# Performance work log

Measured on AMD Instinct MI355X. Metric: run time of the kernel, lower is better.

Reference implementation:

```python
import jax, jax.numpy as jnp
import numpy as np

N = 131072          # total instances
G = 2048            # n_groups
MAX = 128           # padded max group size (>= true max by construction)
E = 256             # embed_dim
H = 8               # num_heads
D = E // H          # head dim


def setup_inputs() -> dict:
    key = jax.random.key(0)
    ks = jax.random.split(key, 9)
    # every group id appears at least once (matches torch.unique-derived groups)
    gids = jnp.concatenate([
        jnp.arange(G, dtype=jnp.int32),
        jax.random.randint(ks[0], (N - G,), 0, G, dtype=jnp.int32),
    ])
    return {
        "tree_preds": jax.random.normal(ks[1], (N, E), dtype=jnp.float32),
        "group_ids": gids,
        "query": jax.random.normal(ks[2], (1, 1, E), dtype=jnp.float32) * 0.02,
        "w_in": jax.random.normal(ks[3], (3 * E, E), dtype=jnp.float32) * 0.02,
        "b_in": jax.random.normal(ks[4], (3 * E,), dtype=jnp.float32) * 0.02,
        "w_out": jax.random.normal(ks[5], (E, E), dtype=jnp.float32) * 0.02,
        "b_out": jax.random.normal(ks[6], (E,), dtype=jnp.float32) * 0.02,
        "w_lin": jax.random.normal(ks[7], (1, E), dtype=jnp.float32) * 0.02,
        "b_lin": jax.random.normal(ks[8], (1,), dtype=jnp.float32) * 0.02,
    }


def _forward(tree_preds, group_ids, query, w_in, b_in, w_out, b_out, w_lin, b_lin):
    # --- scatter ragged groups into padded [G, MAX, E] tensor ---
    sorter = jnp.argsort(group_ids)                   # stable instance sorter
    sorted_gid = group_ids[sorter]
    sizes = jax.ops.segment_sum(jnp.ones_like(group_ids), group_ids,
                                num_segments=G)       # [G] group sizes
    offsets = jnp.cumsum(sizes) - sizes               # exclusive cumsum
    pos = jnp.arange(N, dtype=sizes.dtype) - offsets[sorted_gid]  # slot in group
    embs = jnp.zeros((G, MAX, E), dtype=tree_preds.dtype)
    embs = embs.at[sorted_gid, pos].set(tree_preds[sorter])
    kp_mask = jnp.arange(MAX)[None, :] >= sizes[:, None]          # [G, MAX] True=pad

    # --- single-query multi-head attention pooling ---
    wq, wk, wv = w_in[:E], w_in[E:2 * E], w_in[2 * E:]
    bq, bk, bv = b_in[:E], b_in[E:2 * E], b_in[2 * E:]
    q = (query.reshape(E) @ wq.T + bq).reshape(H, D)              # shared query
    k = (embs @ wk.T + bk).reshape(G, MAX, H, D)
    v = (embs @ wv.T + bv).reshape(G, MAX, H, D)
    scores = jnp.einsum("hd,gmhd->ghm", q, k) / jnp.sqrt(jnp.float32(D))
    scores = jnp.where(kp_mask[:, None, :], -jnp.inf, scores)
    attn = jax.nn.softmax(scores, axis=-1)                        # [G, H, MAX]
    pooled = jnp.einsum("ghm,gmhd->ghd", attn, v).reshape(G, E)
    pooled = pooled @ w_out.T + b_out                             # out_proj
    return pooled @ w_lin.T + b_lin                               # [G, 1]


def reference(tree_preds, group_ids, query, w_in, b_in, w_out, b_out, w_lin, b_lin):
    return _forward(tree_preds, group_ids, query, w_in, b_in,
                    w_out, b_out, w_lin, b_lin)
```

## Files before the change

### kernel.cpp

```cpp
#include <hip/hip_runtime.h>
#include <hip/hip_bf16.h>

#define EDIM 256
#define INV_SQRT_D 0.17677669529663688f
#define FXSCALE 1099511627776.0f

#define WS_QB   4096
#define WS_UB   4104
#define WS_C    4112
#define WS_QS   4128
#define WS_PU   4608
#define WB_BYTE_OFF 36864
#define ZM_BYTE_OFF 65536

typedef __attribute__((ext_vector_type(8))) short short8;
typedef __attribute__((ext_vector_type(4))) float f32x4;

__device__ __forceinline__ unsigned short f2bf(float f) {
  unsigned u = __float_as_uint(f);
  unsigned r = (u + 0x7fffu + ((u >> 16) & 1u)) >> 16;
  return (unsigned short)r;
}

__device__ __forceinline__ unsigned int cvt_pk_bf16(float a, float b) {
  __hip_bfloat162 t = __float22bfloat162_rn(float2{a, b});
  unsigned int u;
  __builtin_memcpy(&u, &t, 4);
  return u;
}

__global__ __launch_bounds__(256) void prep1(
    const float* __restrict__ query, const float* __restrict__ w_in,
    const float* __restrict__ b_in, const float* __restrict__ w_out,
    const float* __restrict__ w_lin, float* __restrict__ ws,
    unsigned long long* __restrict__ zm, int nzm) {
  const int b = blockIdx.x, t = threadIdx.x;
  if (b < 32) {
    const int r = b * 8 + (t >> 5);
    const int l = t & 31;
    const float4 q0 = *(const float4*)(query + l * 8);
    const float4 q1 = *(const float4*)(query + l * 8 + 4);
    const float4 w0 = *(const float4*)(w_in + (size_t)r * EDIM + l * 8);
    const float4 w1 = *(const float4*)(w_in + (size_t)r * EDIM + l * 8 + 4);
    float a = q0.x * w0.x + q0.y * w0.y + q0.z * w0.z + q0.w * w0.w
            + q1.x * w1.x + q1.y * w1.y + q1.z * w1.z + q1.w * w1.w;
    for (int m = 16; m >= 1; m >>= 1) a += __shfl_xor(a, m, 32);
    if (l == 0) ws[WS_QS + r] = a + b_in[r];
  } else if (b < 48) {
    const int k = b - 32;
    float acc = 0.f;
#pragma unroll
    for (int f = 0; f < 16; ++f) {
      const int fr = k * 16 + f;
      acc += w_lin[fr] * w_out[(size_t)fr * EDIM + t];
    }
    ws[WS_PU + k * EDIM + t] = acc;
  } else {
    for (int k = (b - 48) * 256 + t; k < nzm; k += 16 * 256) zm[k] = 0ull;
  }
}

__global__ __launch_bounds__(256) void prep2(
    const float* __restrict__ w_in, const float* __restrict__ b_in,
    const float* __restrict__ b_out, const float* __restrict__ b_lin,
    const float* __restrict__ w_lin, float* __restrict__ ws,
    unsigned short* __restrict__ wb) {
  const int b = blockIdx.x, t = threadIdx.x;
  if (b < 8) {
    __shared__ float qh[32];
    if (t < 32) qh[t] = ws[WS_QS + b * 32 + t];
    __syncthreads();
    float a = 0.f;
#pragma unroll 8
    for (int d = 0; d < 32; ++d)
      a += qh[d] * w_in[(size_t)(EDIM + b * 32 + d) * EDIM + t];
    wb[b * EDIM + t] = f2bf(a * INV_SQRT_D);
  } else if (b < 16) {
    const int j = b - 8;
    __shared__ float uh[32];
    if (t < 32) {
      float s = 0.f;
#pragma unroll
      for (int k = 0; k < 16; ++k) s += ws[WS_PU + k * EDIM + j * 32 + t];
      uh[t] = s;
    }
    __syncthreads();
    float a = 0.f;
#pragma unroll 8
    for (int d = 0; d < 32; ++d)
      a += uh[d] * w_in[(size_t)(2 * EDIM + j * 32 + d) * EDIM + t];
    wb[(8 + j) * EDIM + t] = f2bf(a);
  } else {
    __shared__ float us[EDIM];
    float s = 0.f;
#pragma unroll
    for (int k = 0; k < 16; ++k) s += ws[WS_PU + k * EDIM + t];
    us[t] = s;
    __syncthreads();
    if (t < 8) {
      float qb = 0.f, ub = 0.f;
#pragma unroll 4
      for (int d = 0; d < 32; ++d) {
        qb += ws[WS_QS + t * 32 + d] * b_in[EDIM + t * 32 + d];
        ub += us[t * 32 + d] * b_in[2 * EDIM + t * 32 + d];
      }
      ws[WS_QB + t] = qb * INV_SQRT_D;
      ws[WS_UB + t] = ub;
    }
    if (t == 0) {
      float c = b_lin[0];
      for (int f = 0; f < EDIM; ++f) c += w_lin[f] * b_out[f];
      ws[WS_C] = c;
    }
  }
}

__global__ __launch_bounds__(256, 4) void main_mfma(
    const float* __restrict__ x, const int* __restrict__ gid,
    const float* __restrict__ ws, const unsigned short* __restrict__ wb,
    unsigned long long* __restrict__ zm, int n_items) {
  const int t = threadIdx.x;
  const int lane = t & 63;
  const int n = lane & 15, quad = lane >> 4;
  const int h = n & 7, isw = (n >> 3) & 1;

  short8 bfrag[8];
#pragma unroll
  for (int kc = 0; kc < 8; ++kc)
    bfrag[kc] = *(const short8*)(wb + n * EDIM + quad * 8 + kc * 32);

  const float qb = ws[WS_QB + h];
  const float ub = ws[WS_UB + h];

  const int wid = (int)(blockIdx.x * (blockDim.x >> 6) + (t >> 6));
  const int nw = (int)(gridDim.x * (blockDim.x >> 6));
  const int ntiles = (n_items + 15) >> 4;

  for (int tile = wid; tile < ntiles; tile += nw) {
    const int base = tile << 4;
    const float* rowp = x + (size_t)(base + n) * EDIM + quad * 8;
    f32x4 acc = {0.f, 0.f, 0.f, 0.f};
    int4 g4;
    if (base + 16 <= n_items) {
      g4 = *(const int4*)(gid + base + quad * 4);
#pragma unroll
      for (int kc = 0; kc < 8; ++kc) {
        const float4 v0 = *(const float4*)(rowp + kc * 32);
        const float4 v1 = *(const float4*)(rowp + kc * 32 + 4);
        union { short8 s; unsigned int u[4]; } a;
        a.u[0] = cvt_pk_bf16(v0.x, v0.y);
        a.u[1] = cvt_pk_bf16(v0.z, v0.w);
        a.u[2] = cvt_pk_bf16(v1.x, v1.y);
        a.u[3] = cvt_pk_bf16(v1.z, v1.w);
        acc = __builtin_amdgcn_mfma_f32_16x16x32_bf16(a.s, bfrag[kc], acc, 0, 0, 0);
      }
    } else {
      int gg[4];
#pragma unroll
      for (int r = 0; r < 4; ++r)
        gg[r] = (base + quad * 4 + r < n_items) ? gid[base + quad * 4 + r] : 0;
      g4.x = gg[0]; g4.y = gg[1]; g4.z = gg[2]; g4.w = gg[3];
      const bool live = (base + n < n_items);
#pragma unroll
      for (int kc = 0; kc < 8; ++kc) {
        float4 v0 = {0.f, 0.f, 0.f, 0.f}, v1 = {0.f, 0.f, 0.f, 0.f};
        if (live) {
          v0 = *(const float4*)(rowp + kc * 32);
          v1 = *(const float4*)(rowp + kc * 32 + 4);
        }
        union { short8 s; unsigned int u[4]; } a;
        a.u[0] = cvt_pk_bf16(v0.x, v0.y);
        a.u[1] = cvt_pk_bf16(v0.z, v0.w);
        a.u[2] = cvt_pk_bf16(v1.x, v1.y);
        a.u[3] = cvt_pk_bf16(v1.z, v1.w);
        acc = __builtin_amdgcn_mfma_f32_16x16x32_bf16(a.s, bfrag[kc], acc, 0, 0, 0);
      }
    }
#pragma unroll
    for (int r = 0; r < 4; ++r) {
      const float mine = acc[r];
      const float partner = __shfl_xor(mine, 8, 64);
      const float sv = (isw ? partner : mine) + qb;
      const float wv = (isw ? mine : partner) + ub;
      const float e = __expf(sv);
      const float val = isw ? e * wv : e;
      const int g = (r == 0) ? g4.x : (r == 1) ? g4.y : (r == 2) ? g4.z : g4.w;
      if (base + quad * 4 + r < n_items) {
        const long long qv = llrintf(val * FXSCALE);
        atomicAdd(zm + ((size_t)g * 16 + h * 2 + isw), (unsigned long long)qv);
      }
    }
  }
}

__global__ __launch_bounds__(256) void finalize(
    const long long* __restrict__ zm, const float* __restrict__ ws,
    float* __restrict__ out, int G) {
  const int g = blockIdx.x * blockDim.x + threadIdx.x;
  if (g >= G) return;
  double acc = (double)ws[WS_C];
  const long long* row = zm + (size_t)g * 16;
#pragma unroll
  for (int hh = 0; hh < 8; ++hh)
    acc += (double)row[hh * 2 + 1] / (double)row[hh * 2];
  out[g] = (float)acc;
}

__device__ __forceinline__ float dot16_reduce(const float4 (&W)[16],
                                              const float4 xv, const int lane) {
  float p[16];
#pragma unroll
  for (int j = 0; j < 16; ++j)
    p[j] = W[j].x * xv.x + W[j].y * xv.y + W[j].z * xv.z + W[j].w * xv.w;
#pragma unroll
  for (int j = 0; j < 8; ++j) {
    float send = (lane & 1) ? p[j] : p[j + 8];
    float keep = (lane & 1) ? p[j + 8] : p[j];
    p[j] = keep + __shfl_xor(send, 1, 64);
  }
#pragma unroll
  for (int j = 0; j < 4; ++j) {
    float send = (lane & 2) ? p[j] : p[j + 4];
    float keep = (lane & 2) ? p[j + 4] : p[j];
    p[j] = keep + __shfl_xor(send, 2, 64);
  }
#pragma unroll
  for (int j = 0; j < 2; ++j) {
    float send = (lane & 4) ? p[j] : p[j + 2];
    float keep = (lane & 4) ? p[j + 2] : p[j];
    p[j] = keep + __shfl_xor(send, 4, 64);
  }
  {
    float send = (lane & 8) ? p[0] : p[1];
    float keep = (lane & 8) ? p[1] : p[0];
    p[0] = keep + __shfl_xor(send, 8, 64);
  }
  p[0] += __shfl_xor(p[0], 16, 64);
  p[0] += __shfl_xor(p[0], 32, 64);
  return p[0];
}

__device__ __forceinline__ int bitrev4(const int l4) {
  return ((l4 & 1) << 3) | ((l4 & 2) << 1) | ((l4 & 4) >> 1) | ((l4 & 8) >> 3);
}

__global__ __launch_bounds__(256) void group_scan(
    const float* __restrict__ x, const int* __restrict__ gid,
    const float* __restrict__ query, const float* __restrict__ w_in,
    const float* __restrict__ b_in, const float* __restrict__ w_out,
    const float* __restrict__ b_out, const float* __restrict__ w_lin,
    const float* __restrict__ b_lin, float* __restrict__ out, int n_items) {
  const int g = blockIdx.x;
  const int t = threadIdx.x;
  __shared__ float Wl[16 * EDIM];
  __shared__ float querys[EDIM], wls[EDIM], qs[EDIM], us[EDIM];
  __shared__ float qbias[8], ubias[8], csh;
  __shared__ float part[4][16], sums[16];

  querys[t] = query[t];
  wls[t] = w_lin[t];
  __syncthreads();
  {
    float acc = 0.f;
    const float4* wr = (const float4*)(w_in + (size_t)t * EDIM);
    for (int f4 = 0; f4 < EDIM / 4; ++f4) {
      float4 wv = wr[f4];
      int f = f4 * 4;
      acc += wv.x * querys[f] + wv.y * querys[f + 1] + wv.z * querys[f + 2] + wv.w * querys[f + 3];
    }
    qs[t] = acc + b_in[t];
  }
  {
    float acc = 0.f;
    for (int f = 0; f < EDIM; ++f) acc += wls[f] * w_out[(size_t)f * EDIM + t];
    us[t] = acc;
  }
  __syncthreads();
  for (int j = 0; j < 8; ++j) {
    float a = 0.f;
    for (int d = 0; d < 32; ++d)
      a += qs[j * 32 + d] * w_in[(size_t)(EDIM + j * 32 + d) * EDIM + t];
    Wl[j * EDIM + t] = a * INV_SQRT_D;
  }
  for (int j = 0; j < 8; ++j) {
    float a = 0.f;
    for (int d = 0; d < 32; ++d)
      a += us[j * 32 + d] * w_in[(size_t)(2 * EDIM + j * 32 + d) * EDIM + t];
    Wl[(8 + j) * EDIM + t] = a;
  }
  if (t < 8) {
    float qb = 0.f, ub = 0.f;
    for (int d = 0; d < 32; ++d) {
      qb += qs[t * 32 + d] * b_in[EDIM + t * 32 + d];
      ub += us[t * 32 + d] * b_in[2 * EDIM + t * 32 + d];
    }
    qbias[t] = qb * INV_SQRT_D;
    ubias[t] = ub;
  }
  if (t == 0) {
    float c = b_lin[0];
    for (int f = 0; f < EDIM; ++f) c += wls[f] * b_out[f];
    csh = c;
  }
  __syncthreads();

  const int lane = t & 63;
  const int wave = t >> 6;
  float4 W[16];
#pragma unroll
  for (int j = 0; j < 16; ++j)
    W[j] = *(const float4*)(Wl + j * EDIM + lane * 4);
  const int jv = bitrev4(lane & 15);
  const int h = jv & 7;
  const int isw = (jv >> 3) & 1;
  const float bias_s = qbias[h];
  const float bias_w = ubias[h];

  float accv = 0.f;
  const int nchunk = (n_items + 63) >> 6;
  for (int c = wave; c < nchunk; c += 4) {
    const int i0 = c << 6;
    const int ii = i0 + lane;
    const int gi = (ii < n_items) ? gid[ii] : -1;
    unsigned long long mk = __ballot(gi == g);
    while (mk) {
      const int bpos = __ffsll(mk) - 1;
      mk &= mk - 1;
      const int i = i0 + bpos;
      const float4 xv = *(const float4*)(x + (size_t)i * EDIM + lane * 4);
      const float p0 = dot16_reduce(W, xv, lane);
      const float tpair = __shfl_xor(p0, 1, 64);
      const float sv = (isw ? tpair : p0) + bias_s;
      const float wv = (isw ? p0 : tpair) + bias_w;
      const float e = __expf(sv);
      accv += isw ? e * wv : e;
    }
  }
  if (lane < 16) part[wave][h * 2 + isw] = accv;
  __syncthreads();
  if (t < 16) sums[t] = part[0][t] + part[1][t] + part[2][t] + part[3][t];
  __syncthreads();
  if (t == 0) {
    double acc = (double)csh;
    for (int hh = 0; hh < 8; ++hh)
      acc += (double)sums[2 * hh + 1] / (double)sums[2 * hh];
    out[g] = (float)acc;
  }
}

extern "C" void kernel_launch(void* const* d_in, const int* in_sizes, int n_in,
                              void* d_out, int out_size, void* d_ws, size_t ws_size,
                              hipStream_t stream) {
  const float* tree_preds = (const float*)d_in[0];
  const int* group_ids = (const int*)d_in[1];
  const float* query = (const float*)d_in[2];
  const float* w_in = (const float*)d_in[3];
  const float* b_in = (const float*)d_in[4];
  const float* w_out = (const float*)d_in[5];
  const float* b_out = (const float*)d_in[6];
  const float* w_lin = (const float*)d_in[7];
  const float* b_lin = (const float*)d_in[8];
  float* out = (float*)d_out;

  const int N = in_sizes[1];
  const int G = out_size;

  const size_t needA = (size_t)ZM_BYTE_OFF + (size_t)G * 16 * 8;
  if (ws_size >= needA) {
    float* ws = (float*)d_ws;
    unsigned short* wb = (unsigned short*)((char*)d_ws + WB_BYTE_OFF);
    unsigned long long* zm = (unsigned long long*)((char*)d_ws + ZM_BYTE_OFF);
    prep1<<<64, 256, 0, stream>>>(query, w_in, b_in, w_out, w_lin, ws, zm, G * 16);
    prep2<<<17, 256, 0, stream>>>(w_in, b_in, b_out, b_lin, w_lin, ws, wb);
    main_mfma<<<1024, 256, 0, stream>>>(tree_preds, group_ids, ws, wb, zm, N);
    finalize<<<(G + 255) / 256, 256, 0, stream>>>((const long long*)zm, ws, out, G);
  } else {
    group_scan<<<G, 256, 0, stream>>>(tree_preds, group_ids, query, w_in, b_in,
                                      w_out, b_out, w_lin, b_lin, out, N);
  }
}
```

Baseline: 221.9 us.

## Replace fixed-point 64-bit atomics with float atomics into replicated accumulators

The scatter of per-instance softmax numerators and denominators now uses float atomicAdd instead of converting to 64-bit fixed point and doing integer atomics. Accumulators are replicated NREP=8 times, indexed by block, to spread contention, and finalize sums the replicas before the division. This removes the llrint conversion and halves the atomic payload size while reducing same-address conflicts. In exchange the sums become non-deterministic float sums with lower precision, and the zeroing and finalize work grow with the replica count.

```diff
diff --git a/kernel.cpp b/kernel.cpp
--- a/kernel.cpp
+++ b/kernel.cpp
@@ -3,7 +3,7 @@
 
 #define EDIM 256
 #define INV_SQRT_D 0.17677669529663688f
-#define FXSCALE 1099511627776.0f
+#define NREP 8
 
 #define WS_QB   4096
 #define WS_UB   4104
@@ -118,7 +118,7 @@
 __global__ __launch_bounds__(256, 4) void main_mfma(
     const float* __restrict__ x, const int* __restrict__ gid,
     const float* __restrict__ ws, const unsigned short* __restrict__ wb,
-    unsigned long long* __restrict__ zm, int n_items) {
+    float* __restrict__ zmf, int g16, int n_items) {
   const int t = threadIdx.x;
   const int lane = t & 63;
   const int n = lane & 15, quad = lane >> 4;
@@ -131,6 +131,8 @@
 
   const float qb = ws[WS_QB + h];
   const float ub = ws[WS_UB + h];
+
+  float* __restrict__ zr = zmf + (size_t)(blockIdx.x & (NREP - 1)) * g16;
 
   const int wid = (int)(blockIdx.x * (blockDim.x >> 6) + (t >> 6));
   const int nw = (int)(gridDim.x * (blockDim.x >> 6));
@@ -185,24 +187,34 @@
       const float e = __expf(sv);
       const float val = isw ? e * wv : e;
       const int g = (r == 0) ? g4.x : (r == 1) ? g4.y : (r == 2) ? g4.z : g4.w;
-      if (base + quad * 4 + r < n_items) {
-        const long long qv = llrintf(val * FXSCALE);
-        atomicAdd(zm + ((size_t)g * 16 + h * 2 + isw), (unsigned long long)qv);
-      }
+      if (base + quad * 4 + r < n_items)
+        atomicAdd(zr + ((size_t)g * 16 + h * 2 + isw), val);
     }
   }
 }
 
 __global__ __launch_bounds__(256) void finalize(
-    const long long* __restrict__ zm, const float* __restrict__ ws,
+    const float* __restrict__ zmf, const float* __restrict__ ws,
     float* __restrict__ out, int G) {
   const int g = blockIdx.x * blockDim.x + threadIdx.x;
   if (g >= G) return;
+  float zs[8], ms[8];
+#pragma unroll
+  for (int hh = 0; hh < 8; ++hh) { zs[hh] = 0.f; ms[hh] = 0.f; }
+  const int g16 = G * 16;
+#pragma unroll
+  for (int rep = 0; rep < NREP; ++rep) {
+    const float* row = zmf + (size_t)rep * g16 + (size_t)g * 16;
+#pragma unroll
+    for (int hh = 0; hh < 8; ++hh) {
+      zs[hh] += row[hh * 2];
+      ms[hh] += row[hh * 2 + 1];
+    }
+  }
   double acc = (double)ws[WS_C];
-  const long long* row = zm + (size_t)g * 16;
 #pragma unroll
   for (int hh = 0; hh < 8; ++hh)
-    acc += (double)row[hh * 2 + 1] / (double)row[hh * 2];
+    acc += (double)ms[hh] / (double)zs[hh];
   out[g] = (float)acc;
 }
 
@@ -365,15 +377,17 @@
   const int N = in_sizes[1];
   const int G = out_size;
 
-  const size_t needA = (size_t)ZM_BYTE_OFF + (size_t)G * 16 * 8;
+  const size_t needA = (size_t)ZM_BYTE_OFF + (size_t)NREP * G * 16 * 4;
   if (ws_size >= needA) {
     float* ws = (float*)d_ws;
     unsigned short* wb = (unsigned short*)((char*)d_ws + WB_BYTE_OFF);
-    unsigned long long* zm = (unsigned long long*)((char*)d_ws + ZM_BYTE_OFF);
-    prep1<<<64, 256, 0, stream>>>(query, w_in, b_in, w_out, w_lin, ws, zm, G * 16);
+    float* zmf = (float*)((char*)d_ws + ZM_BYTE_OFF);
+    prep1<<<64, 256, 0, stream>>>(query, w_in, b_in, w_out, w_lin, ws,
+                                  (unsigned long long*)zmf, NREP * G * 8);
     prep2<<<17, 256, 0, stream>>>(w_in, b_in, b_out, b_lin, w_lin, ws, wb);
-    main_mfma<<<1024, 256, 0, stream>>>(tree_preds, group_ids, ws, wb, zm, N);
-    finalize<<<(G + 255) / 256, 256, 0, stream>>>((const long long*)zm, ws, out, G);
+    main_mfma<<<1024, 256, 0, stream>>>(tree_preds, group_ids, ws, wb, zmf,
+                                        G * 16, N);
+    finalize<<<(G + 255) / 256, 256, 0, stream>>>(zmf, ws, out, G);
   } else {
     group_scan<<<G, 256, 0, stream>>>(tree_preds, group_ids, query, w_in, b_in,
                                       w_out, b_out, w_lin, b_lin, out, N);
```

Measured after the change: 222.9 us. No clear change (+0.5%).

## Replace per-item atomic scatter with counting-sort grouping and per-group wave reduction

Applied to the files above, without the earlier changes.

Replaces the streaming MFMA pass, which issued a 64-bit fixed-point atomic per item and head, with a counting sort: a rank kernel (atomic per item on padded counters), a scan inside prep2, and a scatter kernel that builds a permutation. The main kernel then gives each group to one wavefront, which gathers rows through the permutation, reduces softmax numerators and denominators in registers, and writes the output directly, so the finalize kernel goes away. This removes the heavy contention on 64-bit atomics. In exchange it adds two extra launches, random row gathers instead of streaming reads, and load imbalance across groups of different sizes; floating-point summation order also changes.

```diff
diff --git a/kernel.cpp b/kernel.cpp
--- a/kernel.cpp
+++ b/kernel.cpp
@@ -3,7 +3,6 @@
 
 #define EDIM 256
 #define INV_SQRT_D 0.17677669529663688f
-#define FXSCALE 1099511627776.0f
 
 #define WS_QB   4096
 #define WS_UB   4104
@@ -11,7 +10,7 @@
 #define WS_QS   4128
 #define WS_PU   4608
 #define WB_BYTE_OFF 36864
-#define ZM_BYTE_OFF 65536
+#define CNT_BYTE_OFF 65536
 
 typedef __attribute__((ext_vector_type(8))) short short8;
 typedef __attribute__((ext_vector_type(4))) float f32x4;
@@ -27,6 +26,14 @@
   unsigned int u;
   __builtin_memcpy(&u, &t, 4);
   return u;
+}
+
+__device__ __forceinline__ double shfl_xor_dbl(double v, int m) {
+  union { double d; int i[2]; } u;
+  u.d = v;
+  u.i[0] = __shfl_xor(u.i[0], m, 64);
+  u.i[1] = __shfl_xor(u.i[1], m, 64);
+  return u.d;
 }
 
 __global__ __launch_bounds__(256) void prep1(
@@ -60,11 +67,22 @@
   }
 }
 
+__global__ __launch_bounds__(256) void rankk(
+    const int* __restrict__ gid, unsigned* __restrict__ cnt,
+    unsigned* __restrict__ rank, int n_items) {
+  const int i = blockIdx.x * 256 + threadIdx.x;
+  if (i < n_items) {
+    const int g = gid[i];
+    rank[i] = atomicAdd(&cnt[(size_t)g * 16], 1u);
+  }
+}
+
 __global__ __launch_bounds__(256) void prep2(
     const float* __restrict__ w_in, const float* __restrict__ b_in,
     const float* __restrict__ b_out, const float* __restrict__ b_lin,
     const float* __restrict__ w_lin, float* __restrict__ ws,
-    unsigned short* __restrict__ wb) {
+    unsigned short* __restrict__ wb, const unsigned* __restrict__ cnt,
+    unsigned* __restrict__ base, int G) {
   const int b = blockIdx.x, t = threadIdx.x;
   if (b < 8) {
     __shared__ float qh[32];
@@ -90,7 +108,7 @@
     for (int d = 0; d < 32; ++d)
       a += uh[d] * w_in[(size_t)(2 * EDIM + j * 32 + d) * EDIM + t];
     wb[(8 + j) * EDIM + t] = f2bf(a);
-  } else {
+  } else if (b == 16) {
     __shared__ float us[EDIM];
     float s = 0.f;
 #pragma unroll
@@ -112,13 +130,47 @@
       for (int f = 0; f < EDIM; ++f) c += w_lin[f] * b_out[f];
       ws[WS_C] = c;
     }
-  }
-}
-
-__global__ __launch_bounds__(256, 4) void main_mfma(
-    const float* __restrict__ x, const int* __restrict__ gid,
-    const float* __restrict__ ws, const unsigned short* __restrict__ wb,
-    unsigned long long* __restrict__ zm, int n_items) {
+  } else {
+    __shared__ unsigned tsum[256];
+    unsigned c8[8];
+    unsigned s = 0;
+#pragma unroll
+    for (int j = 0; j < 8; ++j) {
+      const int bin = t * 8 + j;
+      c8[j] = (bin < G) ? cnt[(size_t)bin * 16] : 0u;
+      s += c8[j];
+    }
+    tsum[t] = s;
+    __syncthreads();
+    for (int off = 1; off < 256; off <<= 1) {
+      unsigned v = (t >= off) ? tsum[t - off] : 0u;
+      __syncthreads();
+      tsum[t] += v;
+      __syncthreads();
+    }
+    unsigned run = tsum[t] - s;
+#pragma unroll
+    for (int j = 0; j < 8; ++j) {
+      const int bin = t * 8 + j;
+      if (bin <= G) base[bin] = run;
+      run += c8[j];
+    }
+    if (t == 255 && 2048 >= G) base[G] = run;
+  }
+}
+
+__global__ __launch_bounds__(256) void scatterk(
+    const int* __restrict__ gid, const unsigned* __restrict__ rank,
+    const unsigned* __restrict__ base, unsigned* __restrict__ perm,
+    int n_items) {
+  const int i = blockIdx.x * 256 + threadIdx.x;
+  if (i < n_items) perm[base[gid[i]] + rank[i]] = (unsigned)i;
+}
+
+__global__ __launch_bounds__(256, 4) void main_grouped(
+    const float* __restrict__ x, const unsigned* __restrict__ perm,
+    const unsigned* __restrict__ base, const float* __restrict__ ws,
+    const unsigned short* __restrict__ wb, float* __restrict__ out, int G) {
   const int t = threadIdx.x;
   const int lane = t & 63;
   const int n = lane & 15, quad = lane >> 4;
@@ -131,18 +183,26 @@
 
   const float qb = ws[WS_QB + h];
   const float ub = ws[WS_UB + h];
+  const float c = ws[WS_C];
 
   const int wid = (int)(blockIdx.x * (blockDim.x >> 6) + (t >> 6));
   const int nw = (int)(gridDim.x * (blockDim.x >> 6));
-  const int ntiles = (n_items + 15) >> 4;
-
-  for (int tile = wid; tile < ntiles; tile += nw) {
-    const int base = tile << 4;
-    const float* rowp = x + (size_t)(base + n) * EDIM + quad * 8;
-    f32x4 acc = {0.f, 0.f, 0.f, 0.f};
-    int4 g4;
-    if (base + 16 <= n_items) {
-      g4 = *(const int4*)(gid + base + quad * 4);
+
+  for (int g = wid; g < G; g += nw) {
+    const unsigned gb = base[g];
+    const int ng = (int)(base[g + 1] - gb);
+    if (ng <= 0) {
+      if (lane == 0) out[g] = c;
+      continue;
+    }
+    float zsum = 0.f;
+    const int ntile = (ng + 15) >> 4;
+    for (int tt = 0; tt < ntile; ++tt) {
+      const int i0 = tt << 4;
+      const int mrow = i0 + n;
+      const unsigned idx = perm[gb + (unsigned)(mrow < ng ? mrow : ng - 1)];
+      const float* rowp = x + (size_t)idx * EDIM + quad * 8;
+      f32x4 acc = {0.f, 0.f, 0.f, 0.f};
 #pragma unroll
       for (int kc = 0; kc < 8; ++kc) {
         const float4 v0 = *(const float4*)(rowp + kc * 32);
@@ -154,56 +214,27 @@
         a.u[3] = cvt_pk_bf16(v1.z, v1.w);
         acc = __builtin_amdgcn_mfma_f32_16x16x32_bf16(a.s, bfrag[kc], acc, 0, 0, 0);
       }
-    } else {
-      int gg[4];
-#pragma unroll
-      for (int r = 0; r < 4; ++r)
-        gg[r] = (base + quad * 4 + r < n_items) ? gid[base + quad * 4 + r] : 0;
-      g4.x = gg[0]; g4.y = gg[1]; g4.z = gg[2]; g4.w = gg[3];
-      const bool live = (base + n < n_items);
-#pragma unroll
-      for (int kc = 0; kc < 8; ++kc) {
-        float4 v0 = {0.f, 0.f, 0.f, 0.f}, v1 = {0.f, 0.f, 0.f, 0.f};
-        if (live) {
-          v0 = *(const float4*)(rowp + kc * 32);
-          v1 = *(const float4*)(rowp + kc * 32 + 4);
-        }
-        union { short8 s; unsigned int u[4]; } a;
-        a.u[0] = cvt_pk_bf16(v0.x, v0.y);
-        a.u[1] = cvt_pk_bf16(v0.z, v0.w);
-        a.u[2] = cvt_pk_bf16(v1.x, v1.y);
-        a.u[3] = cvt_pk_bf16(v1.z, v1.w);
-        acc = __builtin_amdgcn_mfma_f32_16x16x32_bf16(a.s, bfrag[kc], acc, 0, 0, 0);
+#pragma unroll
+      for (int r = 0; r < 4; ++r) {
+        const float mine = acc[r];
+        const float partner = __shfl_xor(mine, 8, 64);
+        const float sv = (isw ? partner : mine) + qb;
+        const float wv = (isw ? mine : partner) + ub;
+        const float e = __expf(sv);
+        const float val = isw ? e * wv : e;
+        if (i0 + quad * 4 + r < ng) zsum += val;
       }
     }
-#pragma unroll
-    for (int r = 0; r < 4; ++r) {
-      const float mine = acc[r];
-      const float partner = __shfl_xor(mine, 8, 64);
-      const float sv = (isw ? partner : mine) + qb;
-      const float wv = (isw ? mine : partner) + ub;
-      const float e = __expf(sv);
-      const float val = isw ? e * wv : e;
-      const int g = (r == 0) ? g4.x : (r == 1) ? g4.y : (r == 2) ? g4.z : g4.w;
-      if (base + quad * 4 + r < n_items) {
-        const long long qv = llrintf(val * FXSCALE);
-        atomicAdd(zm + ((size_t)g * 16 + h * 2 + isw), (unsigned long long)qv);
-      }
-    }
-  }
-}
-
-__global__ __launch_bounds__(256) void finalize(
-    const long long* __restrict__ zm, const float* __restrict__ ws,
-    float* __restrict__ out, int G) {
-  const int g = blockIdx.x * blockDim.x + threadIdx.x;
-  if (g >= G) return;
-  double acc = (double)ws[WS_C];
-  const long long* row = zm + (size_t)g * 16;
-#pragma unroll
-  for (int hh = 0; hh < 8; ++hh)
-    acc += (double)row[hh * 2 + 1] / (double)row[hh * 2];
-  out[g] = (float)acc;
+    zsum += __shfl_xor(zsum, 16, 64);
+    zsum += __shfl_xor(zsum, 32, 64);
+    const float partner = __shfl_xor(zsum, 8, 64);
+    double dr = 0.0;
+    if (!isw) dr = (double)partner / (double)zsum;
+    dr += shfl_xor_dbl(dr, 1);
+    dr += shfl_xor_dbl(dr, 2);
+    dr += shfl_xor_dbl(dr, 4);
+    if (lane == 0) out[g] = (float)((double)c + dr);
+  }
 }
 
 __device__ __forceinline__ float dot16_reduce(const float4 (&W)[16],
@@ -365,15 +396,27 @@
   const int N = in_sizes[1];
   const int G = out_size;
 
-  const size_t needA = (size_t)ZM_BYTE_OFF + (size_t)G * 16 * 8;
-  if (ws_size >= needA) {
+  const size_t cnt_off = CNT_BYTE_OFF;
+  const size_t base_off = cnt_off + (size_t)G * 16 * 4;
+  const size_t rank_off = (base_off + (size_t)(G + 1) * 4 + 255) & ~(size_t)255;
+  const size_t perm_off = (rank_off + (size_t)N * 4 + 255) & ~(size_t)255;
+  const size_t needA = perm_off + (size_t)N * 4;
+
+  if (ws_size >= needA && G <= 2048) {
     float* ws = (float*)d_ws;
     unsigned short* wb = (unsigned short*)((char*)d_ws + WB_BYTE_OFF);
-    unsigned long long* zm = (unsigned long long*)((char*)d_ws + ZM_BYTE_OFF);
-    prep1<<<64, 256, 0, stream>>>(query, w_in, b_in, w_out, w_lin, ws, zm, G * 16);
-    prep2<<<17, 256, 0, stream>>>(w_in, b_in, b_out, b_lin, w_lin, ws, wb);
-    main_mfma<<<1024, 256, 0, stream>>>(tree_preds, group_ids, ws, wb, zm, N);
-    finalize<<<(G + 255) / 256, 256, 0, stream>>>((const long long*)zm, ws, out, G);
+    unsigned* cnt = (unsigned*)((char*)d_ws + cnt_off);
+    unsigned* basep = (unsigned*)((char*)d_ws + base_off);
+    unsigned* rank = (unsigned*)((char*)d_ws + rank_off);
+    unsigned* perm = (unsigned*)((char*)d_ws + perm_off);
+
+    prep1<<<64, 256, 0, stream>>>(query, w_in, b_in, w_out, w_lin, ws,
+                                  (unsigned long long*)cnt, G * 8);
+    rankk<<<(N + 255) / 256, 256, 0, stream>>>(group_ids, cnt, rank, N);
+    prep2<<<18, 256, 0, stream>>>(w_in, b_in, b_out, b_lin, w_lin, ws, wb,
+                                  cnt, basep, G);
+    scatterk<<<(N + 255) / 256, 256, 0, stream>>>(group_ids, rank, basep, perm, N);
+    main_grouped<<<512, 256, 0, stream>>>(tree_preds, perm, basep, ws, wb, out, G);
   } else {
     group_scan<<<G, 256, 0, stream>>>(tree_preds, group_ids, query, w_in, b_in,
                                       w_out, b_out, w_lin, b_lin, out, N);
```

New measurement: 237.3 us. +6.9%, slower.
